# Performance work log

Measured on AMD Instinct MI355X. Metric: run time of the kernel, lower is better.

Reference implementation:

```python
import jax, jax.numpy as jnp
import numpy as np

TAU = 0.07
EPS = 1e-12  # matches torch F.normalize default eps


def setup_inputs() -> dict:
    key = jax.random.key(0)
    k1, k2 = jax.random.split(key)
    B, C, H, W, K = 4, 256, 256, 256, 19
    feat = jax.random.normal(k1, (B, C, H, W), dtype=jnp.float32)
    # binary ground-truth one-hot-ish masks; gt.eq(1) selects positives
    gt = jax.random.randint(k2, (B, K, H, W), 0, 2).astype(jnp.float32)
    return {"feat": feat, "gt": gt}


def _l2norm(x, axis):
    n = jnp.sqrt(jnp.sum(x * x, axis=axis, keepdims=True))
    return x / jnp.maximum(n, EPS)


def reference(feat, gt):
    # feat: [B,C,H,W], gt: [B,K,H,W] binary
    pos = (gt == 1.0).astype(feat.dtype)              # [B,K,H,W]
    fnorm = _l2norm(feat, axis=1)                     # per-pixel L2 normalize over C
    # scatter-add normalized features into class prototypes
    k0 = jnp.einsum('bkhw,bchw->kc', pos, fnorm)      # [K,C]
    k0n = _l2norm(k0, axis=1)                         # [K,C]
    # prototype-vs-pixel similarities, softmax over classes
    logits = jnp.einsum('kc,bchw->bkhw', k0n, fnorm) / TAU  # [B,K,H,W]
    logp = jax.nn.log_softmax(logits, axis=1)
    num_pos = jnp.sum(pos)
    loss = -jnp.sum(pos * logp) / num_pos
    return loss
```

## Files before the change

kernel.cpp:

```cpp
#include <hip/hip_runtime.h>
#include <math.h>

namespace {
constexpr int Cn = 256;
constexpr int Kn = 19;
constexpr int HW = 256 * 256;
constexpr int P  = 4 * HW;
constexpr float TAUv = 0.07f;
constexpr float EPSv = 1e-12f;

constexpr int K0_OFF   = 0;
constexpr int K0N_OFF  = 4864;
constexpr int SUMS_OFF = 9728;
constexpr int ZERO_N   = 9730;
constexpr int P1_GRID  = 1024;
constexpr int P3_GRID  = P / 512;
}

__device__ __forceinline__ float bcast_f(float x) {
  return __uint_as_float((unsigned)__builtin_amdgcn_readfirstlane((int)__float_as_uint(x)));
}
__device__ __forceinline__ unsigned bcast_u(unsigned x) {
  return (unsigned)__builtin_amdgcn_readfirstlane((int)x);
}

__global__ __launch_bounds__(256) void gc_init(float* __restrict__ ws) {
  int i = blockIdx.x * 256 + threadIdx.x;
  if (i < ZERO_N) ws[i] = 0.0f;
}

__global__ __launch_bounds__(256, 4) void gc_phase1(const float* __restrict__ feat,
                                                    const float* __restrict__ gt,
                                                    float* __restrict__ k0) {
  __shared__ float tile[32 * 256];
  __shared__ float part2[32][33];
  __shared__ float rnL[32];
  __shared__ unsigned mskL[32];

  const int t  = threadIdx.x;
  const int pq = t & 7;
  const int g  = t >> 3;

  float acc[Kn];
#pragma unroll
  for (int k = 0; k < Kn; k++) acc[k] = 0.0f;

  for (int tid = blockIdx.x; tid < P / 32; tid += gridDim.x) {
    const int p0  = tid << 5;
    const int b   = p0 >> 16;
    const int hw0 = p0 & (HW - 1);
    const float* fb = feat + (size_t)b * (Cn * HW) + hw0;

    __syncthreads();

    float4 v4[8];
#pragma unroll
    for (int j = 0; j < 8; j++)
      v4[j] = *(const float4*)&fb[(size_t)((g << 3) + j) * HW + (pq << 2)];

    float ps0 = 0.f, ps1 = 0.f, ps2 = 0.f, ps3 = 0.f;
#pragma unroll
    for (int j = 0; j < 8; j++) {
      const int c  = (g << 3) + j;
      const int px = pq << 2;
      ps0 = fmaf(v4[j].x, v4[j].x, ps0);
      ps1 = fmaf(v4[j].y, v4[j].y, ps1);
      ps2 = fmaf(v4[j].z, v4[j].z, ps2);
      ps3 = fmaf(v4[j].w, v4[j].w, ps3);
      tile[((px + 0) << 8) + (c ^ (px + 0))] = v4[j].x;
      tile[((px + 1) << 8) + (c ^ (px + 1))] = v4[j].y;
      tile[((px + 2) << 8) + (c ^ (px + 2))] = v4[j].z;
      tile[((px + 3) << 8) + (c ^ (px + 3))] = v4[j].w;
    }
    part2[(pq << 2) + 0][g] = ps0;
    part2[(pq << 2) + 1][g] = ps1;
    part2[(pq << 2) + 2][g] = ps2;
    part2[(pq << 2) + 3][g] = ps3;

    unsigned msk = 0;
    if (t < 32) {
      const float* gb = gt + (size_t)b * (Kn * HW) + hw0 + t;
#pragma unroll
      for (int k = 0; k < Kn; k++)
        msk |= (gb[(size_t)k * HW] == 1.0f) ? (1u << k) : 0u;
    }

    __syncthreads();

    if (t < 32) {
      float fss = 0.0f;
#pragma unroll
      for (int gg = 0; gg < 32; gg++) fss += part2[t][gg];
      rnL[t]  = 1.0f / fmaxf(sqrtf(fss), EPSv);
      mskL[t] = msk;
    }

    __syncthreads();

#pragma unroll 8
    for (int pp = 0; pp < 32; pp++) {
      const float    rn = bcast_f(rnL[pp]);
      const unsigned mk = bcast_u(mskL[pp]);
      const float    fv = tile[(pp << 8) + (t ^ pp)];
#pragma unroll
      for (int k = 0; k < Kn; k++) {
        const float w = ((mk >> k) & 1u) ? rn : 0.0f;
        acc[k] = fmaf(fv, w, acc[k]);
      }
    }
  }

#pragma unroll
  for (int k = 0; k < Kn; k++) atomicAdd(&k0[k * 256 + t], acc[k]);
}

__global__ __launch_bounds__(256) void gc_phase2(const float* __restrict__ k0,
                                                 float* __restrict__ k0n) {
  const int lane = threadIdx.x & 63;
  const int wv   = threadIdx.x >> 6;
  for (int r = wv; r < Kn; r += 4) {
    float s = 0.0f;
#pragma unroll
    for (int j = 0; j < 4; j++) {
      const float v = k0[r * 256 + (j << 6) + lane];
      s += v * v;
    }
#pragma unroll
    for (int off = 32; off > 0; off >>= 1) s += __shfl_down(s, off);
    s = __shfl(s, 0);
    const float rn = 1.0f / fmaxf(sqrtf(s), EPSv);
#pragma unroll
    for (int j = 0; j < 4; j++) {
      const int c = (j << 6) + lane;
      k0n[r * 256 + c] = k0[r * 256 + c] * rn;
    }
  }
}

__device__ __forceinline__ void p3_load4(float4 (&dst)[8],
                                         const float* __restrict__ fb, int base) {
#pragma unroll
  for (int j = 0; j < 8; j++)
    dst[j] = *(const float4*)&fb[(size_t)(base + j) * HW];
}

__device__ __forceinline__ void p3_compute4(const float4 (&v)[8], int c0,
                                            const float* __restrict__ k0n,
                                            float (&dot)[Kn][4], float (&ss)[4]) {
#pragma unroll
  for (int j4 = 0; j4 < 8; j4 += 4) {
    const float4 f0 = v[j4 + 0], f1 = v[j4 + 1];
    const float4 f2 = v[j4 + 2], f3 = v[j4 + 3];
    ss[0] = fmaf(f0.x, f0.x, ss[0]); ss[0] = fmaf(f1.x, f1.x, ss[0]);
    ss[0] = fmaf(f2.x, f2.x, ss[0]); ss[0] = fmaf(f3.x, f3.x, ss[0]);
    ss[1] = fmaf(f0.y, f0.y, ss[1]); ss[1] = fmaf(f1.y, f1.y, ss[1]);
    ss[1] = fmaf(f2.y, f2.y, ss[1]); ss[1] = fmaf(f3.y, f3.y, ss[1]);
    ss[2] = fmaf(f0.z, f0.z, ss[2]); ss[2] = fmaf(f1.z, f1.z, ss[2]);
    ss[2] = fmaf(f2.z, f2.z, ss[2]); ss[2] = fmaf(f3.z, f3.z, ss[2]);
    ss[3] = fmaf(f0.w, f0.w, ss[3]); ss[3] = fmaf(f1.w, f1.w, ss[3]);
    ss[3] = fmaf(f2.w, f2.w, ss[3]); ss[3] = fmaf(f3.w, f3.w, ss[3]);
#pragma unroll
    for (int k = 0; k < Kn; k++) {
      const float4 w = *(const float4*)(k0n + k * 256 + c0 + j4);
      dot[k][0] = fmaf(f3.x, w.w, fmaf(f2.x, w.z, fmaf(f1.x, w.y, fmaf(f0.x, w.x, dot[k][0]))));
      dot[k][1] = fmaf(f3.y, w.w, fmaf(f2.y, w.z, fmaf(f1.y, w.y, fmaf(f0.y, w.x, dot[k][1]))));
      dot[k][2] = fmaf(f3.z, w.w, fmaf(f2.z, w.z, fmaf(f1.z, w.y, fmaf(f0.z, w.x, dot[k][2]))));
      dot[k][3] = fmaf(f3.w, w.w, fmaf(f2.w, w.z, fmaf(f1.w, w.y, fmaf(f0.w, w.x, dot[k][3]))));
    }
  }
}

__global__ __launch_bounds__(128, 2) void gc_phase3(const float* __restrict__ feat,
                                                    const float* __restrict__ gt,
                                                    const float* __restrict__ k0n,
                                                    float* __restrict__ sums) {
  const int t    = threadIdx.x;
  const int pix0 = blockIdx.x << 9;
  const int b    = pix0 >> 16;
  const int hw   = (pix0 & (HW - 1)) + (t << 2);
  const float* fb = feat + (size_t)b * (Cn * HW) + hw;

  float dot[Kn][4];
#pragma unroll
  for (int k = 0; k < Kn; k++)
#pragma unroll
    for (int i = 0; i < 4; i++) dot[k][i] = 0.0f;
  float ss[4] = {0.f, 0.f, 0.f, 0.f};

  float4 va[8], vb[8];
  p3_load4(va, fb, 0);
  for (int c0 = 0; c0 < Cn; c0 += 16) {
    p3_load4(vb, fb, c0 + 8);
    p3_compute4(va, c0, k0n, dot, ss);
    if (c0 + 16 < Cn) p3_load4(va, fb, c0 + 16);
    p3_compute4(vb, c0 + 8, k0n, dot, ss);
  }

  const float* gb = gt + (size_t)b * (Kn * HW) + hw;
  float4 gv[Kn];
#pragma unroll
  for (int k = 0; k < Kn; k++) gv[k] = *(const float4*)&gb[(size_t)k * HW];

  float lsum = 0.0f, npos = 0.0f;
#pragma unroll
  for (int i = 0; i < 4; i++) {
    const float sc = 1.0f / (fmaxf(sqrtf(ss[i]), EPSv) * TAUv);
    float mx = -1e30f;
    float d[Kn];
#pragma unroll
    for (int k = 0; k < Kn; k++) { d[k] = dot[k][i] * sc; mx = fmaxf(mx, d[k]); }
    float se = 0.0f;
#pragma unroll
    for (int k = 0; k < Kn; k++) se += __expf(d[k] - mx);
    const float lse = __logf(se) + mx;
#pragma unroll
    for (int k = 0; k < Kn; k++) {
      const float gvi = (i == 0) ? gv[k].x : (i == 1) ? gv[k].y : (i == 2) ? gv[k].z : gv[k].w;
      if (gvi == 1.0f) { lsum += lse - d[k]; npos += 1.0f; }
    }
  }

#pragma unroll
  for (int off = 32; off > 0; off >>= 1) {
    lsum += __shfl_down(lsum, off);
    npos += __shfl_down(npos, off);
  }
  if ((t & 63) == 0) {
    atomicAdd(&sums[0], lsum);
    atomicAdd(&sums[1], npos);
  }
}

__global__ void gc_finalize(const float* __restrict__ sums, float* __restrict__ out) {
  if (threadIdx.x == 0 && blockIdx.x == 0)
    out[0] = sums[0] / sums[1];
}

extern "C" void kernel_launch(void* const* d_in, const int* in_sizes, int n_in,
                              void* d_out, int out_size, void* d_ws, size_t ws_size,
                              hipStream_t stream) {
  const float* feat = (const float*)d_in[0];
  const float* gt   = (const float*)d_in[1];
  float* ws  = (float*)d_ws;
  float* out = (float*)d_out;

  float* k0   = ws + K0_OFF;
  float* k0n  = ws + K0N_OFF;
  float* sums = ws + SUMS_OFF;

  gc_init<<<dim3((ZERO_N + 255) / 256), dim3(256), 0, stream>>>(ws);
  gc_phase1<<<dim3(P1_GRID), dim3(256), 0, stream>>>(feat, gt, k0);
  gc_phase2<<<dim3(1), dim3(256), 0, stream>>>(k0, k0n);
  gc_phase3<<<dim3(P3_GRID), dim3(128), 0, stream>>>(feat, gt, k0n, sums);
  gc_finalize<<<dim3(1), dim3(64), 0, stream>>>(sums, out);
}
```

Baseline: 549.4 us.

## Prefetch next feature tile in phase1, refine LDS swizzle, deepen phase3 loads

In phase1, the feature loads for the next tile are issued before the scatter-accumulate loop over the current tile, so global memory latency overlaps with compute. The LDS write/read swizzle gains an extra XOR term to cut bank conflicts. In phase3, the double-buffered channel chunk grows from 8 to 16 float4s per buffer, putting more loads in flight at the cost of more registers and possibly lower occupancy.

```diff
diff --git a/kernel.cpp b/kernel.cpp
--- a/kernel.cpp
+++ b/kernel.cpp
@@ -40,42 +40,48 @@
   const int t  = threadIdx.x;
   const int pq = t & 7;
   const int g  = t >> 3;
+  const int px = pq << 2;
 
   float acc[Kn];
 #pragma unroll
   for (int k = 0; k < Kn; k++) acc[k] = 0.0f;
 
-  for (int tid = blockIdx.x; tid < P / 32; tid += gridDim.x) {
+  int tid = blockIdx.x;
+  float4 v4[8];
+  {
     const int p0  = tid << 5;
     const int b   = p0 >> 16;
     const int hw0 = p0 & (HW - 1);
     const float* fb = feat + (size_t)b * (Cn * HW) + hw0;
+#pragma unroll
+    for (int j = 0; j < 8; j++)
+      v4[j] = *(const float4*)&fb[(size_t)((g << 3) + j) * HW + px];
+  }
+
+  while (tid < P / 32) {
+    const int p0  = tid << 5;
+    const int b   = p0 >> 16;
+    const int hw0 = p0 & (HW - 1);
 
     __syncthreads();
 
-    float4 v4[8];
-#pragma unroll
-    for (int j = 0; j < 8; j++)
-      v4[j] = *(const float4*)&fb[(size_t)((g << 3) + j) * HW + (pq << 2)];
-
     float ps0 = 0.f, ps1 = 0.f, ps2 = 0.f, ps3 = 0.f;
 #pragma unroll
     for (int j = 0; j < 8; j++) {
-      const int c  = (g << 3) + j;
-      const int px = pq << 2;
+      const int c = (g << 3) + j;
       ps0 = fmaf(v4[j].x, v4[j].x, ps0);
       ps1 = fmaf(v4[j].y, v4[j].y, ps1);
       ps2 = fmaf(v4[j].z, v4[j].z, ps2);
       ps3 = fmaf(v4[j].w, v4[j].w, ps3);
-      tile[((px + 0) << 8) + (c ^ (px + 0))] = v4[j].x;
-      tile[((px + 1) << 8) + (c ^ (px + 1))] = v4[j].y;
-      tile[((px + 2) << 8) + (c ^ (px + 2))] = v4[j].z;
-      tile[((px + 3) << 8) + (c ^ (px + 3))] = v4[j].w;
-    }
-    part2[(pq << 2) + 0][g] = ps0;
-    part2[(pq << 2) + 1][g] = ps1;
-    part2[(pq << 2) + 2][g] = ps2;
-    part2[(pq << 2) + 3][g] = ps3;
+      tile[((px + 0) << 8) + (c ^ (px + 0) ^ pq)] = v4[j].x;
+      tile[((px + 1) << 8) + (c ^ (px + 1) ^ pq)] = v4[j].y;
+      tile[((px + 2) << 8) + (c ^ (px + 2) ^ pq)] = v4[j].z;
+      tile[((px + 3) << 8) + (c ^ (px + 3) ^ pq)] = v4[j].w;
+    }
+    part2[px + 0][g] = ps0;
+    part2[px + 1][g] = ps1;
+    part2[px + 2][g] = ps2;
+    part2[px + 3][g] = ps3;
 
     unsigned msk = 0;
     if (t < 32) {
@@ -96,18 +102,31 @@
     }
 
     __syncthreads();
+
+    const int ntid = tid + gridDim.x;
+    if (ntid < P / 32) {
+      const int np0  = ntid << 5;
+      const int nb   = np0 >> 16;
+      const int nhw0 = np0 & (HW - 1);
+      const float* nfb = feat + (size_t)nb * (Cn * HW) + nhw0;
+#pragma unroll
+      for (int j = 0; j < 8; j++)
+        v4[j] = *(const float4*)&nfb[(size_t)((g << 3) + j) * HW + px];
+    }
 
 #pragma unroll 8
     for (int pp = 0; pp < 32; pp++) {
       const float    rn = bcast_f(rnL[pp]);
       const unsigned mk = bcast_u(mskL[pp]);
-      const float    fv = tile[(pp << 8) + (t ^ pp)];
+      const float    fv = tile[(pp << 8) + (t ^ pp ^ (pp >> 2))];
 #pragma unroll
       for (int k = 0; k < Kn; k++) {
         const float w = ((mk >> k) & 1u) ? rn : 0.0f;
         acc[k] = fmaf(fv, w, acc[k]);
       }
     }
+
+    tid = ntid;
   }
 
 #pragma unroll
@@ -137,18 +156,18 @@
   }
 }
 
-__device__ __forceinline__ void p3_load4(float4 (&dst)[8],
-                                         const float* __restrict__ fb, int base) {
-#pragma unroll
-  for (int j = 0; j < 8; j++)
+__device__ __forceinline__ void p3_load16(float4 (&dst)[16],
+                                          const float* __restrict__ fb, int base) {
+#pragma unroll
+  for (int j = 0; j < 16; j++)
     dst[j] = *(const float4*)&fb[(size_t)(base + j) * HW];
 }
 
-__device__ __forceinline__ void p3_compute4(const float4 (&v)[8], int c0,
-                                            const float* __restrict__ k0n,
-                                            float (&dot)[Kn][4], float (&ss)[4]) {
-#pragma unroll
-  for (int j4 = 0; j4 < 8; j4 += 4) {
+__device__ __forceinline__ void p3_compute16(const float4 (&v)[16], int c0,
+                                             const float* __restrict__ k0n,
+                                             float (&dot)[Kn][4], float (&ss)[4]) {
+#pragma unroll
+  for (int j4 = 0; j4 < 16; j4 += 4) {
     const float4 f0 = v[j4 + 0], f1 = v[j4 + 1];
     const float4 f2 = v[j4 + 2], f3 = v[j4 + 3];
     ss[0] = fmaf(f0.x, f0.x, ss[0]); ss[0] = fmaf(f1.x, f1.x, ss[0]);
@@ -187,13 +206,13 @@
     for (int i = 0; i < 4; i++) dot[k][i] = 0.0f;
   float ss[4] = {0.f, 0.f, 0.f, 0.f};
 
-  float4 va[8], vb[8];
-  p3_load4(va, fb, 0);
-  for (int c0 = 0; c0 < Cn; c0 += 16) {
-    p3_load4(vb, fb, c0 + 8);
-    p3_compute4(va, c0, k0n, dot, ss);
-    if (c0 + 16 < Cn) p3_load4(va, fb, c0 + 16);
-    p3_compute4(vb, c0 + 8, k0n, dot, ss);
+  float4 va[16], vb[16];
+  p3_load16(va, fb, 0);
+  for (int c0 = 0; c0 < Cn; c0 += 32) {
+    p3_load16(vb, fb, c0 + 16);
+    p3_compute16(va, c0, k0n, dot, ss);
+    if (c0 + 32 < Cn) p3_load16(va, fb, c0 + 32);
+    p3_compute16(vb, c0 + 16, k0n, dot, ss);
   }
 
   const float* gb = gt + (size_t)b * (Kn * HW) + hw;
```

Measured after the change: 631.9 us. 15.0% more time.

## Double-buffer phase1 tiles with prefetch and shrink phase3 per-thread pixel count

Applied to the files above, without the earlier changes.

Phase1 now processes 16-pixel tiles with double-buffered shared memory. It prefetches the next tile's features and gt masks into registers while the current tile is accumulated, which drops one barrier per iteration. It also reduces the per-pixel norm partials with wave shuffles instead of a shared 32x33 array. Phase3 handles 2 pixels per thread instead of 4 and doubles the grid, lowering register pressure to raise occupancy at the cost of more k0n loads per pixel.

```diff
diff --git a/kernel.cpp b/kernel.cpp
--- a/kernel.cpp
+++ b/kernel.cpp
@@ -9,19 +9,15 @@
 constexpr float TAUv = 0.07f;
 constexpr float EPSv = 1e-12f;
 
+constexpr int TPX = 16;
+constexpr int NT  = P / TPX;
+
 constexpr int K0_OFF   = 0;
 constexpr int K0N_OFF  = 4864;
 constexpr int SUMS_OFF = 9728;
 constexpr int ZERO_N   = 9730;
 constexpr int P1_GRID  = 1024;
-constexpr int P3_GRID  = P / 512;
-}
-
-__device__ __forceinline__ float bcast_f(float x) {
-  return __uint_as_float((unsigned)__builtin_amdgcn_readfirstlane((int)__float_as_uint(x)));
-}
-__device__ __forceinline__ unsigned bcast_u(unsigned x) {
-  return (unsigned)__builtin_amdgcn_readfirstlane((int)x);
+constexpr int P3_GRID  = P / 256;
 }
 
 __global__ __launch_bounds__(256) void gc_init(float* __restrict__ ws) {
@@ -29,85 +25,105 @@
   if (i < ZERO_N) ws[i] = 0.0f;
 }
 
+__device__ __forceinline__ void p1_load(float4 (&v4)[4], float (&gtv)[Kn],
+                                        const float* __restrict__ feat,
+                                        const float* __restrict__ gt,
+                                        int tid, int t, int g, int pq) {
+  const int p0  = tid << 4;
+  const int b   = p0 >> 16;
+  const int hw0 = p0 & (HW - 1);
+  const float* fb = feat + (size_t)b * (Cn * HW) + hw0;
+#pragma unroll
+  for (int j = 0; j < 4; j++)
+    v4[j] = *(const float4*)&fb[(size_t)((g << 2) + j) * HW + (pq << 2)];
+  if (t < TPX) {
+    const float* gb = gt + (size_t)b * (Kn * HW) + hw0 + t;
+#pragma unroll
+    for (int k = 0; k < Kn; k++) gtv[k] = gb[(size_t)k * HW];
+  }
+}
+
 __global__ __launch_bounds__(256, 4) void gc_phase1(const float* __restrict__ feat,
                                                     const float* __restrict__ gt,
                                                     float* __restrict__ k0) {
-  __shared__ float tile[32 * 256];
-  __shared__ float part2[32][33];
-  __shared__ float rnL[32];
-  __shared__ unsigned mskL[32];
-
-  const int t  = threadIdx.x;
-  const int pq = t & 7;
-  const int g  = t >> 3;
+  __shared__ float tile[2][TPX * 256];
+  __shared__ float swpf[2][TPX][4];
+  __shared__ unsigned mskI[2][TPX];
+
+  const int t    = threadIdx.x;
+  const int pq   = t & 3;
+  const int g    = t >> 2;
+  const int lane = t & 63;
+  const int wv   = t >> 6;
 
   float acc[Kn];
 #pragma unroll
   for (int k = 0; k < Kn; k++) acc[k] = 0.0f;
 
-  for (int tid = blockIdx.x; tid < P / 32; tid += gridDim.x) {
-    const int p0  = tid << 5;
-    const int b   = p0 >> 16;
-    const int hw0 = p0 & (HW - 1);
-    const float* fb = feat + (size_t)b * (Cn * HW) + hw0;
-
-    __syncthreads();
-
-    float4 v4[8];
-#pragma unroll
-    for (int j = 0; j < 8; j++)
-      v4[j] = *(const float4*)&fb[(size_t)((g << 3) + j) * HW + (pq << 2)];
-
+  int tid = blockIdx.x;
+  float4 v4[4];
+  float  gtv[Kn];
+  p1_load(v4, gtv, feat, gt, tid, t, g, pq);
+
+  int cur = 0;
+  while (tid < NT) {
     float ps0 = 0.f, ps1 = 0.f, ps2 = 0.f, ps3 = 0.f;
-#pragma unroll
-    for (int j = 0; j < 8; j++) {
-      const int c  = (g << 3) + j;
-      const int px = pq << 2;
+    const int px = pq << 2;
+#pragma unroll
+    for (int j = 0; j < 4; j++) {
+      const int c = (g << 2) + j;
       ps0 = fmaf(v4[j].x, v4[j].x, ps0);
       ps1 = fmaf(v4[j].y, v4[j].y, ps1);
       ps2 = fmaf(v4[j].z, v4[j].z, ps2);
       ps3 = fmaf(v4[j].w, v4[j].w, ps3);
-      tile[((px + 0) << 8) + (c ^ (px + 0))] = v4[j].x;
-      tile[((px + 1) << 8) + (c ^ (px + 1))] = v4[j].y;
-      tile[((px + 2) << 8) + (c ^ (px + 2))] = v4[j].z;
-      tile[((px + 3) << 8) + (c ^ (px + 3))] = v4[j].w;
-    }
-    part2[(pq << 2) + 0][g] = ps0;
-    part2[(pq << 2) + 1][g] = ps1;
-    part2[(pq << 2) + 2][g] = ps2;
-    part2[(pq << 2) + 3][g] = ps3;
-
-    unsigned msk = 0;
-    if (t < 32) {
-      const float* gb = gt + (size_t)b * (Kn * HW) + hw0 + t;
+      tile[cur][((px + 0) << 8) + (c ^ pq)] = v4[j].x;
+      tile[cur][((px + 1) << 8) + (c ^ pq)] = v4[j].y;
+      tile[cur][((px + 2) << 8) + (c ^ pq)] = v4[j].z;
+      tile[cur][((px + 3) << 8) + (c ^ pq)] = v4[j].w;
+    }
+#pragma unroll
+    for (int m = 4; m <= 32; m <<= 1) {
+      ps0 += __shfl_xor(ps0, m);
+      ps1 += __shfl_xor(ps1, m);
+      ps2 += __shfl_xor(ps2, m);
+      ps3 += __shfl_xor(ps3, m);
+    }
+    if (lane < 4) {
+      swpf[cur][(lane << 2) + 0][wv] = ps0;
+      swpf[cur][(lane << 2) + 1][wv] = ps1;
+      swpf[cur][(lane << 2) + 2][wv] = ps2;
+      swpf[cur][(lane << 2) + 3][wv] = ps3;
+    }
+    if (t < TPX) {
+      unsigned m = 0;
 #pragma unroll
       for (int k = 0; k < Kn; k++)
-        msk |= (gb[(size_t)k * HW] == 1.0f) ? (1u << k) : 0u;
+        m |= (gtv[k] == 1.0f) ? (1u << k) : 0u;
+      mskI[cur][t] = m;
     }
 
     __syncthreads();
 
-    if (t < 32) {
-      float fss = 0.0f;
-#pragma unroll
-      for (int gg = 0; gg < 32; gg++) fss += part2[t][gg];
-      rnL[t]  = 1.0f / fmaxf(sqrtf(fss), EPSv);
-      mskL[t] = msk;
-    }
-
-    __syncthreads();
-
-#pragma unroll 8
-    for (int pp = 0; pp < 32; pp++) {
-      const float    rn = bcast_f(rnL[pp]);
-      const unsigned mk = bcast_u(mskL[pp]);
-      const float    fv = tile[(pp << 8) + (t ^ pp)];
+    const int ntid = tid + P1_GRID;
+    if (ntid < NT) p1_load(v4, gtv, feat, gt, ntid, t, g, pq);
+
+#pragma unroll 4
+    for (int pp = 0; pp < TPX; pp++) {
+      const float4 sp = *(const float4*)&swpf[cur][pp][0];
+      const float fss = ((sp.x + sp.y) + sp.z) + sp.w;
+      const float rn  = 1.0f / fmaxf(sqrtf(fss), EPSv);
+      const unsigned mk = mskI[cur][pp];
+      const float fv  = tile[cur][(pp << 8) + (t ^ (pp >> 2))];
+      const float fvn = fv * rn;
 #pragma unroll
       for (int k = 0; k < Kn; k++) {
-        const float w = ((mk >> k) & 1u) ? rn : 0.0f;
-        acc[k] = fmaf(fv, w, acc[k]);
+        const float bf = (float)((mk >> k) & 1u);
+        acc[k] = fmaf(fvn, bf, acc[k]);
       }
     }
+
+    tid = ntid;
+    cur ^= 1;
   }
 
 #pragma unroll
@@ -137,35 +153,29 @@
   }
 }
 
-__device__ __forceinline__ void p3_load4(float4 (&dst)[8],
+__device__ __forceinline__ void p3_load8(float2 (&dst)[8],
                                          const float* __restrict__ fb, int base) {
 #pragma unroll
   for (int j = 0; j < 8; j++)
-    dst[j] = *(const float4*)&fb[(size_t)(base + j) * HW];
-}
-
-__device__ __forceinline__ void p3_compute4(const float4 (&v)[8], int c0,
-                                            const float* __restrict__ k0n,
-                                            float (&dot)[Kn][4], float (&ss)[4]) {
+    dst[j] = *(const float2*)&fb[(size_t)(base + j) * HW];
+}
+
+__device__ __forceinline__ void p3_comp8(const float2 (&v)[8], int c0,
+                                         const float* __restrict__ k0n,
+                                         float (&dot)[Kn][2], float (&ss)[2]) {
 #pragma unroll
   for (int j4 = 0; j4 < 8; j4 += 4) {
-    const float4 f0 = v[j4 + 0], f1 = v[j4 + 1];
-    const float4 f2 = v[j4 + 2], f3 = v[j4 + 3];
+    const float2 f0 = v[j4 + 0], f1 = v[j4 + 1];
+    const float2 f2 = v[j4 + 2], f3 = v[j4 + 3];
     ss[0] = fmaf(f0.x, f0.x, ss[0]); ss[0] = fmaf(f1.x, f1.x, ss[0]);
     ss[0] = fmaf(f2.x, f2.x, ss[0]); ss[0] = fmaf(f3.x, f3.x, ss[0]);
     ss[1] = fmaf(f0.y, f0.y, ss[1]); ss[1] = fmaf(f1.y, f1.y, ss[1]);
     ss[1] = fmaf(f2.y, f2.y, ss[1]); ss[1] = fmaf(f3.y, f3.y, ss[1]);
-    ss[2] = fmaf(f0.z, f0.z, ss[2]); ss[2] = fmaf(f1.z, f1.z, ss[2]);
-    ss[2] = fmaf(f2.z, f2.z, ss[2]); ss[2] = fmaf(f3.z, f3.z, ss[2]);
-    ss[3] = fmaf(f0.w, f0.w, ss[3]); ss[3] = fmaf(f1.w, f1.w, ss[3]);
-    ss[3] = fmaf(f2.w, f2.w, ss[3]); ss[3] = fmaf(f3.w, f3.w, ss[3]);
 #pragma unroll
     for (int k = 0; k < Kn; k++) {
       const float4 w = *(const float4*)(k0n + k * 256 + c0 + j4);
       dot[k][0] = fmaf(f3.x, w.w, fmaf(f2.x, w.z, fmaf(f1.x, w.y, fmaf(f0.x, w.x, dot[k][0]))));
       dot[k][1] = fmaf(f3.y, w.w, fmaf(f2.y, w.z, fmaf(f1.y, w.y, fmaf(f0.y, w.x, dot[k][1]))));
-      dot[k][2] = fmaf(f3.z, w.w, fmaf(f2.z, w.z, fmaf(f1.z, w.y, fmaf(f0.z, w.x, dot[k][2]))));
-      dot[k][3] = fmaf(f3.w, w.w, fmaf(f2.w, w.z, fmaf(f1.w, w.y, fmaf(f0.w, w.x, dot[k][3]))));
     }
   }
 }
@@ -175,35 +185,33 @@
                                                     const float* __restrict__ k0n,
                                                     float* __restrict__ sums) {
   const int t    = threadIdx.x;
-  const int pix0 = blockIdx.x << 9;
+  const int pix0 = blockIdx.x << 8;
   const int b    = pix0 >> 16;
-  const int hw   = (pix0 & (HW - 1)) + (t << 2);
+  const int hw   = (pix0 & (HW - 1)) + (t << 1);
   const float* fb = feat + (size_t)b * (Cn * HW) + hw;
 
-  float dot[Kn][4];
-#pragma unroll
-  for (int k = 0; k < Kn; k++)
-#pragma unroll
-    for (int i = 0; i < 4; i++) dot[k][i] = 0.0f;
-  float ss[4] = {0.f, 0.f, 0.f, 0.f};
-
-  float4 va[8], vb[8];
-  p3_load4(va, fb, 0);
+  float dot[Kn][2];
+#pragma unroll
+  for (int k = 0; k < Kn; k++) { dot[k][0] = 0.0f; dot[k][1] = 0.0f; }
+  float ss[2] = {0.f, 0.f};
+
+  float2 va[8], vb[8];
+  p3_load8(va, fb, 0);
   for (int c0 = 0; c0 < Cn; c0 += 16) {
-    p3_load4(vb, fb, c0 + 8);
-    p3_compute4(va, c0, k0n, dot, ss);
-    if (c0 + 16 < Cn) p3_load4(va, fb, c0 + 16);
-    p3_compute4(vb, c0 + 8, k0n, dot, ss);
+    p3_load8(vb, fb, c0 + 8);
+    p3_comp8(va, c0, k0n, dot, ss);
+    if (c0 + 16 < Cn) p3_load8(va, fb, c0 + 16);
+    p3_comp8(vb, c0 + 8, k0n, dot, ss);
   }
 
   const float* gb = gt + (size_t)b * (Kn * HW) + hw;
-  float4 gv[Kn];
-#pragma unroll
-  for (int k = 0; k < Kn; k++) gv[k] = *(const float4*)&gb[(size_t)k * HW];
+  float2 gv[Kn];
+#pragma unroll
+  for (int k = 0; k < Kn; k++) gv[k] = *(const float2*)&gb[(size_t)k * HW];
 
   float lsum = 0.0f, npos = 0.0f;
 #pragma unroll
-  for (int i = 0; i < 4; i++) {
+  for (int i = 0; i < 2; i++) {
     const float sc = 1.0f / (fmaxf(sqrtf(ss[i]), EPSv) * TAUv);
     float mx = -1e30f;
     float d[Kn];
@@ -215,7 +223,7 @@
     const float lse = __logf(se) + mx;
 #pragma unroll
     for (int k = 0; k < Kn; k++) {
-      const float gvi = (i == 0) ? gv[k].x : (i == 1) ? gv[k].y : (i == 2) ? gv[k].z : gv[k].w;
+      const float gvi = (i == 0) ? gv[k].x : gv[k].y;
       if (gvi == 1.0f) { lsum += lse - d[k]; npos += 1.0f; }
     }
   }
```

Result: no change. 539.0 us (-1.9%).
